# Kernel optimization log

Hardware: AMD Instinct MI355X
Metric: run time of the kernel (lower is better)

The kernel has to match this reference:

```python
import jax, jax.numpy as jnp
import numpy as np

NEG_INF = -1e9  # same masked_fill constant as the torch module
ALPHA = 0.1     # LeakyReLU negative slope


def setup_inputs() -> dict:
    key = jax.random.key(0)
    k1, k2, k3, k4, k5 = jax.random.split(key, 5)
    B, N, Din, Dout = 8, 2048, 512, 512
    features = jax.random.normal(k1, (B, N, Din), dtype=jnp.float32)
    graph = jax.random.randint(k2, (B, N, N), 0, 2, dtype=jnp.int64)
    # xavier_uniform with gain=1.414: limit = gain*sqrt(6/(fan_in+fan_out))
    lim_w = 1.414 * np.sqrt(6.0 / (Din + Dout))
    w = jax.random.uniform(k3, (Din, Dout), jnp.float32, -lim_w, lim_w)
    lim_a = 1.414 * np.sqrt(6.0 / (Dout + 1))
    a1 = jax.random.uniform(k4, (Dout, 1), jnp.float32, -lim_a, lim_a)
    a2 = jax.random.uniform(k5, (Dout, 1), jnp.float32, -lim_a, lim_a)
    return {"features": features, "graph": graph, "w": w, "a1": a1, "a2": a2}


def reference(features, graph, w, a1, a2):
    # hidden: [B, N, Dout]
    hidden = jnp.einsum("bni,io->bno", features, w)
    s1 = hidden @ a1  # [B, N, 1] -> broadcasts over columns
    s2 = hidden @ a2  # [B, N, 1] -> transposed broadcasts over rows
    # e[b,i,j] = leaky_relu(s1[b,i] + s2[b,j])
    e = jax.nn.leaky_relu(s1 + jnp.swapaxes(s2, 1, 2), negative_slope=ALPHA)
    e = jnp.where(graph == 0, NEG_INF, e)
    attn = jax.nn.softmax(e, axis=-1)  # [B, N, N]; dropout p=0 -> identity
    h_prime = jnp.einsum("bij,bjo->bio", attn, hidden)
    return jax.nn.elu(h_prime)  # concat=True
```

## Files before the change

### kernel.cpp

```cpp
#include <hip/hip_runtime.h>
#include <math.h>

#define B_ 8
#define N_ 2048
#define D_ 512
#define NROWS (B_ * N_)
#define NEG_ALPHA 0.1f

typedef __bf16 bf16;
typedef __bf16 bf16x4 __attribute__((ext_vector_type(4)));
typedef __bf16 bf16x8 __attribute__((ext_vector_type(8)));
typedef float f32x4 __attribute__((ext_vector_type(4)));
typedef float f32x16 __attribute__((ext_vector_type(16)));

__global__ __launch_bounds__(256) void k_prep(const float* __restrict__ W,
                                              bf16* __restrict__ Wt) {
  const int dout = blockIdx.x;
  const int t = threadIdx.x;
#pragma unroll
  for (int p = 0; p < 2; ++p) {
    int din = t + p * 256;
    Wt[dout * D_ + din] = (bf16)W[din * D_ + dout];
  }
}

__global__ __launch_bounds__(256) void k_wa(const float* __restrict__ W,
                                            const float* __restrict__ a1,
                                            const float* __restrict__ a2,
                                            float* __restrict__ wa1,
                                            float* __restrict__ wa2) {
  const int wv = threadIdx.x >> 6, lane = threadIdx.x & 63;
  const int row = blockIdx.x * 4 + wv;
  const float* wr = W + (size_t)row * D_;
  float d1 = 0.f, d2 = 0.f;
#pragma unroll
  for (int p = 0; p < 8; ++p) {
    int c = lane + p * 64;
    float w = wr[c];
    d1 = fmaf(w, a1[c], d1);
    d2 = fmaf(w, a2[c], d2);
  }
#pragma unroll
  for (int off = 32; off > 0; off >>= 1) {
    d1 += __shfl_down(d1, off, 64);
    d2 += __shfl_down(d2, off, 64);
  }
  if (lane == 0) {
    wa1[row] = d1;
    wa2[row] = d2;
  }
}

__global__ __launch_bounds__(256) void k_scores_x(const float* __restrict__ X,
                                                  const float* __restrict__ wa1,
                                                  const float* __restrict__ wa2,
                                                  float* __restrict__ s1,
                                                  float* __restrict__ s2) {
  const int wv = threadIdx.x >> 6, lane = threadIdx.x & 63;
  const int r = blockIdx.x * 4 + wv;
  const float* x = X + (size_t)r * D_;
  float d1 = 0.f, d2 = 0.f;
#pragma unroll
  for (int p = 0; p < 2; ++p) {
    int c = lane * 4 + p * 256;
    float4 xv = *(const float4*)&x[c];
    float4 w1 = *(const float4*)&wa1[c];
    float4 w2 = *(const float4*)&wa2[c];
    d1 += xv.x * w1.x + xv.y * w1.y + xv.z * w1.z + xv.w * w1.w;
    d2 += xv.x * w2.x + xv.y * w2.y + xv.z * w2.z + xv.w * w2.w;
  }
#pragma unroll
  for (int off = 32; off > 0; off >>= 1) {
    d1 += __shfl_down(d1, off, 64);
    d2 += __shfl_down(d2, off, 64);
  }
  if (lane == 0) {
    s1[r] = d1;
    s2[r] = d2;
  }
}

#define LDH 40

__global__ __launch_bounds__(256, 2) void k_hiddenT(const float* __restrict__ X,
                                                    const bf16* __restrict__ Wt,
                                                    bf16* __restrict__ Ht) {
  __shared__ bf16 As[128][LDH];
  __shared__ bf16 Bs[128][LDH];
  const int t = threadIdx.x;
  const int m0 = blockIdx.y * 128;
  const int n0 = blockIdx.x * 128;
  const int lane = t & 63, w = t >> 6;
  const int wm = w >> 1, wn = w & 1;
  const int l15 = lane & 15, q = lane >> 4;

  f32x4 acc[4][4];
#pragma unroll
  for (int i = 0; i < 4; ++i)
#pragma unroll
    for (int j = 0; j < 4; ++j) acc[i][j] = (f32x4){0.f, 0.f, 0.f, 0.f};

  bf16x8 av[2];
  float4 bv[4];
#pragma unroll
  for (int p = 0; p < 2; ++p) {
    int s = t + p * 256;
    av[p] = *(const bf16x8*)&Wt[(size_t)(m0 + (s >> 2)) * D_ + (s & 3) * 8];
  }
#pragma unroll
  for (int p = 0; p < 4; ++p) {
    int s = t + p * 256;
    bv[p] = *(const float4*)&X[(size_t)(n0 + (s >> 3)) * D_ + (s & 7) * 4];
  }

  for (int k0 = 0; k0 < D_; k0 += 32) {
    __syncthreads();
#pragma unroll
    for (int p = 0; p < 2; ++p) {
      int s = t + p * 256;
      *(bf16x8*)&As[s >> 2][(s & 3) * 8] = av[p];
    }
#pragma unroll
    for (int p = 0; p < 4; ++p) {
      int s = t + p * 256;
      float4 v = bv[p];
      bf16x4 h = {(bf16)v.x, (bf16)v.y, (bf16)v.z, (bf16)v.w};
      *(bf16x4*)&Bs[s >> 3][(s & 7) * 4] = h;
    }
    __syncthreads();
    if (k0 + 32 < D_) {
#pragma unroll
      for (int p = 0; p < 2; ++p) {
        int s = t + p * 256;
        av[p] = *(const bf16x8*)&Wt[(size_t)(m0 + (s >> 2)) * D_ + k0 + 32 + (s & 3) * 8];
      }
#pragma unroll
      for (int p = 0; p < 4; ++p) {
        int s = t + p * 256;
        bv[p] = *(const float4*)&X[(size_t)(n0 + (s >> 3)) * D_ + k0 + 32 + (s & 7) * 4];
      }
    }
    bf16x8 a[4], bb[4];
#pragma unroll
    for (int i = 0; i < 4; ++i)
      a[i] = *(const bf16x8*)&As[wm * 64 + i * 16 + l15][q * 8];
#pragma unroll
    for (int j = 0; j < 4; ++j)
      bb[j] = *(const bf16x8*)&Bs[wn * 64 + j * 16 + l15][q * 8];
#pragma unroll
    for (int i = 0; i < 4; ++i)
#pragma unroll
      for (int j = 0; j < 4; ++j)
        acc[i][j] =
            __builtin_amdgcn_mfma_f32_16x16x32_bf16(a[i], bb[j], acc[i][j], 0, 0, 0);
  }
#pragma unroll
  for (int i = 0; i < 4; ++i)
#pragma unroll
    for (int r = 0; r < 4; ++r) {
      int dout = m0 + wm * 64 + i * 16 + q * 4 + r;
#pragma unroll
      for (int j = 0; j < 4; ++j) {
        int row = n0 + wn * 64 + j * 16 + l15;
        Ht[(size_t)dout * NROWS + row] = (bf16)acc[i][j][r];
      }
    }
}

#define AT_BM 64
#define AT_BK 64
#define LDP 72

__global__ __launch_bounds__(512, 1) void k_attn(const bf16* __restrict__ Ht,
                                                 const int* __restrict__ graph,
                                                 const float* __restrict__ s1,
                                                 const float* __restrict__ s2,
                                                 float* __restrict__ out) {
  __shared__ bf16 Hs[D_][LDP];
  __shared__ bf16 Ps[AT_BM][LDP];
  __shared__ float s2s[N_];
  __shared__ float sum_part[AT_BM][8];
  __shared__ float row_sum[AT_BM];

  const int t = threadIdx.x;
  const int b = blockIdx.y;
  const int i0 = blockIdx.x * AT_BM;
  const int lane = t & 63, w = t >> 6;
  const int r31 = lane & 31, half = lane >> 5;

  const bf16* Htb = Ht + (size_t)b * N_;
  const int* Gb = graph + ((size_t)b * N_ + i0) * N_;

  for (int c = t; c < N_; c += 512) s2s[c] = s2[b * N_ + c];

  const int pi = t >> 3;
  const int pj = (t & 7) * 8;
  const float s1r = s1[b * N_ + i0 + pi];
  float rsum = 0.f;

  f32x16 acc[2][2];
#pragma unroll
  for (int i = 0; i < 2; ++i)
#pragma unroll
    for (int j = 0; j < 2; ++j)
#pragma unroll
      for (int r = 0; r < 16; ++r) acc[i][j][r] = 0.f;

  bf16x8 hv[8];
  int4 g0, g1;
#pragma unroll
  for (int p = 0; p < 8; ++p) {
    int s = t + p * 512;
    hv[p] = *(const bf16x8*)&Htb[(size_t)(s >> 3) * NROWS + (s & 7) * 8];
  }
  g0 = *(const int4*)&Gb[(size_t)pi * N_ + pj];
  g1 = *(const int4*)&Gb[(size_t)pi * N_ + pj + 4];

  __syncthreads();

  for (int j0 = 0; j0 < N_; j0 += AT_BK) {
    float pv[8];
    {
      int gg[8] = {g0.x, g0.y, g0.z, g0.w, g1.x, g1.y, g1.z, g1.w};
#pragma unroll
      for (int q = 0; q < 8; ++q) {
        float e = s1r + s2s[j0 + pj + q];
        e = (e > 0.f) ? e : NEG_ALPHA * e;
        pv[q] = (gg[q] != 0) ? __expf(e) : 0.f;
        rsum += pv[q];
      }
    }
    __syncthreads();
#pragma unroll
    for (int p = 0; p < 8; ++p) {
      int s = t + p * 512;
      *(bf16x8*)&Hs[s >> 3][(s & 7) * 8] = hv[p];
    }
    {
      bf16x8 pb = {(bf16)pv[0], (bf16)pv[1], (bf16)pv[2], (bf16)pv[3],
                   (bf16)pv[4], (bf16)pv[5], (bf16)pv[6], (bf16)pv[7]};
      *(bf16x8*)&Ps[pi][pj] = pb;
    }
    __syncthreads();
    if (j0 + AT_BK < N_) {
#pragma unroll
      for (int p = 0; p < 8; ++p) {
        int s = t + p * 512;
        hv[p] = *(const bf16x8*)&Htb[(size_t)(s >> 3) * NROWS + j0 + AT_BK + (s & 7) * 8];
      }
      g0 = *(const int4*)&Gb[(size_t)pi * N_ + j0 + AT_BK + pj];
      g1 = *(const int4*)&Gb[(size_t)pi * N_ + j0 + AT_BK + pj + 4];
    }
#pragma unroll
    for (int ks = 0; ks < 4; ++ks) {
      const int ko = ks * 16 + half * 8;
      bf16x8 a0 = *(const bf16x8*)&Ps[r31][ko];
      bf16x8 a1 = *(const bf16x8*)&Ps[32 + r31][ko];
      bf16x8 b0 = *(const bf16x8*)&Hs[w * 64 + r31][ko];
      bf16x8 b1 = *(const bf16x8*)&Hs[w * 64 + 32 + r31][ko];
      acc[0][0] = __builtin_amdgcn_mfma_f32_32x32x16_bf16(a0, b0, acc[0][0], 0, 0, 0);
      acc[0][1] = __builtin_amdgcn_mfma_f32_32x32x16_bf16(a0, b1, acc[0][1], 0, 0, 0);
      acc[1][0] = __builtin_amdgcn_mfma_f32_32x32x16_bf16(a1, b0, acc[1][0], 0, 0, 0);
      acc[1][1] = __builtin_amdgcn_mfma_f32_32x32x16_bf16(a1, b1, acc[1][1], 0, 0, 0);
    }
  }

  sum_part[pi][t & 7] = rsum;
  __syncthreads();
  if (t < AT_BM) {
    float s = 0.f;
#pragma unroll
    for (int k = 0; k < 8; ++k) s += sum_part[t][k];
    row_sum[t] = s;
  }
  __syncthreads();

#pragma unroll
  for (int mt = 0; mt < 2; ++mt) {
    float inv[16];
#pragma unroll
    for (int r = 0; r < 16; ++r)
      inv[r] = 1.f / row_sum[mt * 32 + (r & 3) + 8 * (r >> 2) + 4 * half];
#pragma unroll
    for (int nt = 0; nt < 2; ++nt) {
      const int d = w * 64 + nt * 32 + r31;
#pragma unroll
      for (int r = 0; r < 16; ++r) {
        int i = mt * 32 + (r & 3) + 8 * (r >> 2) + 4 * half;
        float x = acc[mt][nt][r] * inv[r];
        out[((size_t)b * N_ + i0 + i) * D_ + d] = (x > 0.f) ? x : expm1f(x);
      }
    }
  }
}

extern "C" void kernel_launch(void* const* d_in, const int* in_sizes, int n_in,
                              void* d_out, int out_size, void* d_ws,
                              size_t ws_size, hipStream_t stream) {
  const float* X = (const float*)d_in[0];
  const int* graph = (const int*)d_in[1];
  const float* W = (const float*)d_in[2];
  const float* a1 = (const float*)d_in[3];
  const float* a2 = (const float*)d_in[4];
  float* out = (float*)d_out;

  char* ws = (char*)d_ws;
  bf16* Wt = (bf16*)ws;
  bf16* Ht = (bf16*)(ws + (1 << 19));
  float* s1 = (float*)(ws + (1 << 19) + (16 << 20));
  float* s2 = s1 + NROWS;
  float* wa1 = s2 + NROWS;
  float* wa2 = wa1 + D_;

  hipLaunchKernelGGL(k_prep, dim3(512), dim3(256), 0, stream, W, Wt);
  hipLaunchKernelGGL(k_wa, dim3(128), dim3(256), 0, stream, W, a1, a2, wa1, wa2);
  hipLaunchKernelGGL(k_scores_x, dim3(NROWS / 4), dim3(256), 0, stream, X, wa1,
                     wa2, s1, s2);
  hipLaunchKernelGGL(k_hiddenT, dim3(NROWS / 128, D_ / 128), dim3(256), 0,
                     stream, X, Wt, Ht);
  hipLaunchKernelGGL(k_attn, dim3(N_ / AT_BM, B_), dim3(512), 0, stream, Ht,
                     graph, s1, s2, out);
}
```

Before: 298.8 us.

## Read H operands directly from global in attention kernel, double-buffer P tile

Removes the shared-memory staging of the 512x64 H tile: each wave now loads its MFMA B operands straight from global (L2-cached) memory, and the P tile is double-buffered so one barrier per iteration suffices. Shrinking LDS and dropping the min-blocks launch bound allows more blocks per CU. The grid is flattened with batch interleaved across block IDs so that concurrent blocks share the same H batch in cache. The trade-off is more global/L2 traffic, since each block re-reads H without LDS reuse across waves, and the next graph tile is prefetched only one iteration ahead.

```diff
diff --git a/kernel.cpp b/kernel.cpp
--- a/kernel.cpp
+++ b/kernel.cpp
@@ -171,20 +171,20 @@
 #define AT_BK 64
 #define LDP 72
 
-__global__ __launch_bounds__(512, 1) void k_attn(const bf16* __restrict__ Ht,
-                                                 const int* __restrict__ graph,
-                                                 const float* __restrict__ s1,
-                                                 const float* __restrict__ s2,
-                                                 float* __restrict__ out) {
-  __shared__ bf16 Hs[D_][LDP];
-  __shared__ bf16 Ps[AT_BM][LDP];
+__global__ __launch_bounds__(512) void k_attn(const bf16* __restrict__ Ht,
+                                              const int* __restrict__ graph,
+                                              const float* __restrict__ s1,
+                                              const float* __restrict__ s2,
+                                              float* __restrict__ out) {
+  __shared__ __align__(16) bf16 Ps[2][AT_BM][LDP];
   __shared__ float s2s[N_];
   __shared__ float sum_part[AT_BM][8];
   __shared__ float row_sum[AT_BM];
 
   const int t = threadIdx.x;
-  const int b = blockIdx.y;
-  const int i0 = blockIdx.x * AT_BM;
+  const int bid = blockIdx.x;
+  const int b = bid & 7;
+  const int i0 = (bid >> 3) * AT_BM;
   const int lane = t & 63, w = t >> 6;
   const int r31 = lane & 31, half = lane >> 5;
 
@@ -206,63 +206,57 @@
 #pragma unroll
       for (int r = 0; r < 16; ++r) acc[i][j][r] = 0.f;
 
-  bf16x8 hv[8];
-  int4 g0, g1;
-#pragma unroll
-  for (int p = 0; p < 8; ++p) {
-    int s = t + p * 512;
-    hv[p] = *(const bf16x8*)&Htb[(size_t)(s >> 3) * NROWS + (s & 7) * 8];
-  }
-  g0 = *(const int4*)&Gb[(size_t)pi * N_ + pj];
-  g1 = *(const int4*)&Gb[(size_t)pi * N_ + pj + 4];
+  int4 g0 = *(const int4*)&Gb[(size_t)pi * N_ + pj];
+  int4 g1 = *(const int4*)&Gb[(size_t)pi * N_ + pj + 4];
 
   __syncthreads();
 
-  for (int j0 = 0; j0 < N_; j0 += AT_BK) {
+#pragma unroll 1
+  for (int it = 0; it < N_ / AT_BK; ++it) {
+    const int j0 = it * AT_BK;
+    int jn = j0 + AT_BK;
+    if (jn >= N_) jn = 0;
+    int4 n0_ = *(const int4*)&Gb[(size_t)pi * N_ + jn + pj];
+    int4 n1_ = *(const int4*)&Gb[(size_t)pi * N_ + jn + pj + 4];
+
     float pv[8];
     {
       int gg[8] = {g0.x, g0.y, g0.z, g0.w, g1.x, g1.y, g1.z, g1.w};
+      f32x4 sA = *(const f32x4*)&s2s[j0 + pj];
+      f32x4 sB = *(const f32x4*)&s2s[j0 + pj + 4];
+      float sv[8] = {sA.x, sA.y, sA.z, sA.w, sB.x, sB.y, sB.z, sB.w};
 #pragma unroll
       for (int q = 0; q < 8; ++q) {
-        float e = s1r + s2s[j0 + pj + q];
+        float e = s1r + sv[q];
         e = (e > 0.f) ? e : NEG_ALPHA * e;
         pv[q] = (gg[q] != 0) ? __expf(e) : 0.f;
         rsum += pv[q];
       }
     }
-    __syncthreads();
-#pragma unroll
-    for (int p = 0; p < 8; ++p) {
-      int s = t + p * 512;
-      *(bf16x8*)&Hs[s >> 3][(s & 7) * 8] = hv[p];
-    }
+    const int cur = it & 1;
     {
       bf16x8 pb = {(bf16)pv[0], (bf16)pv[1], (bf16)pv[2], (bf16)pv[3],
                    (bf16)pv[4], (bf16)pv[5], (bf16)pv[6], (bf16)pv[7]};
-      *(bf16x8*)&Ps[pi][pj] = pb;
+      *(bf16x8*)&Ps[cur][pi][pj] = pb;
     }
     __syncthreads();
-    if (j0 + AT_BK < N_) {
-#pragma unroll
-      for (int p = 0; p < 8; ++p) {
-        int s = t + p * 512;
-        hv[p] = *(const bf16x8*)&Htb[(size_t)(s >> 3) * NROWS + j0 + AT_BK + (s & 7) * 8];
-      }
-      g0 = *(const int4*)&Gb[(size_t)pi * N_ + j0 + AT_BK + pj];
-      g1 = *(const int4*)&Gb[(size_t)pi * N_ + j0 + AT_BK + pj + 4];
-    }
+
+    const bf16* Hw0 = Htb + (size_t)(w * 64 + r31) * NROWS + j0;
+    const bf16* Hw1 = Htb + (size_t)(w * 64 + 32 + r31) * NROWS + j0;
 #pragma unroll
     for (int ks = 0; ks < 4; ++ks) {
       const int ko = ks * 16 + half * 8;
-      bf16x8 a0 = *(const bf16x8*)&Ps[r31][ko];
-      bf16x8 a1 = *(const bf16x8*)&Ps[32 + r31][ko];
-      bf16x8 b0 = *(const bf16x8*)&Hs[w * 64 + r31][ko];
-      bf16x8 b1 = *(const bf16x8*)&Hs[w * 64 + 32 + r31][ko];
+      bf16x8 a0 = *(const bf16x8*)&Ps[cur][r31][ko];
+      bf16x8 a1 = *(const bf16x8*)&Ps[cur][32 + r31][ko];
+      bf16x8 b0 = *(const bf16x8*)&Hw0[ko];
+      bf16x8 b1 = *(const bf16x8*)&Hw1[ko];
       acc[0][0] = __builtin_amdgcn_mfma_f32_32x32x16_bf16(a0, b0, acc[0][0], 0, 0, 0);
       acc[0][1] = __builtin_amdgcn_mfma_f32_32x32x16_bf16(a0, b1, acc[0][1], 0, 0, 0);
       acc[1][0] = __builtin_amdgcn_mfma_f32_32x32x16_bf16(a1, b0, acc[1][0], 0, 0, 0);
       acc[1][1] = __builtin_amdgcn_mfma_f32_32x32x16_bf16(a1, b1, acc[1][1], 0, 0, 0);
     }
+    g0 = n0_;
+    g1 = n1_;
   }
 
   sum_part[pi][t & 7] = rsum;
@@ -318,6 +312,6 @@
                      wa2, s1, s2);
   hipLaunchKernelGGL(k_hiddenT, dim3(NROWS / 128, D_ / 128), dim3(256), 0,
                      stream, X, Wt, Ht);
-  hipLaunchKernelGGL(k_attn, dim3(N_ / AT_BM, B_), dim3(512), 0, stream, Ht,
+  hipLaunchKernelGGL(k_attn, dim3(N_ / AT_BM * B_), dim3(512), 0, stream, Ht,
                      graph, s1, s2, out);
 }
```

Measured after the change: 300.7 us. About the same (+0.7%).
